# Performance work log

Measured on AMD Instinct MI355X. Metric: run time of the kernel, lower is better.

Reference implementation:

```python
import jax, jax.numpy as jnp
import numpy as np

FWD_W = 1.0
BWD_W = 1.0
EPS = 1e-12  # guard sqrt gradient at exact zero


def setup_inputs() -> dict:
    key = jax.random.key(0)
    k1, k2 = jax.random.split(key)
    pred = jax.random.normal(k1, (4, 8192, 3), dtype=jnp.float32)
    target = jax.random.normal(k2, (4, 8192, 3), dtype=jnp.float32)
    return {"pred": pred, "target": target}


def reference(pred, target):
    # pairwise Euclidean distances (torch.cdist, p=2): (B, N, M)
    sq = (jnp.sum(pred * pred, axis=-1)[:, :, None]
          + jnp.sum(target * target, axis=-1)[:, None, :]
          - 2.0 * jnp.einsum('bnd,bmd->bnm', pred, target))
    dist = jnp.sqrt(jnp.maximum(sq, EPS))
    forward_dist = jnp.min(dist, axis=2)   # (B, N): pred -> nearest target
    backward_dist = jnp.min(dist, axis=1)  # (B, M): target -> nearest pred
    total = FWD_W * jnp.sum(forward_dist, axis=1) + BWD_W * jnp.sum(backward_dist, axis=1)
    return jnp.mean(total)  # reduction='mean'
```

## Files before the change

kernel.cpp:

```cpp
#include <hip/hip_runtime.h>
#include <math.h>

#define BATCH   4
#define NPTS    8192
#define THREADS 256
#define QPT     8
#define QPB     (THREADS * QPT)
#define QBLK    (NPTS / QPB)
#define NSLICE  32
#define SLICE   (NPTS / NSLICE)

typedef float v2f __attribute__((ext_vector_type(2)));

__device__ __forceinline__ v2f pk_fma(v2f a, v2f b, v2f c) {
    v2f d;
    asm("v_pk_fma_f32 %0, %1, %2, %3" : "=v"(d) : "v"(a), "v"(b), "v"(c));
    return d;
}

__global__ __launch_bounds__(THREADS)
void chamfer_min_kernel(const float* __restrict__ pred,
                        const float* __restrict__ target,
                        unsigned int* __restrict__ minbits)
{
    __shared__ float4 sdb[SLICE * 2];

    const int tid = threadIdx.x;
    const int bid = blockIdx.x;
    const int s   = bid & (NSLICE - 1);
    const int qb  = (bid >> 5) & (QBLK - 1);
    const int b   = (bid >> 7) & 3;
    const int dir = bid >> 9;

    const float* __restrict__ qsrc = (dir == 0) ? pred : target;
    const float* __restrict__ dsrc = (dir == 0) ? target : pred;

    {
        const float* dbase = dsrc + ((size_t)b * NPTS + (size_t)s * SLICE) * 3;
        const float x = dbase[3 * tid + 0];
        const float y = dbase[3 * tid + 1];
        const float z = dbase[3 * tid + 2];
        const float w = fmaf(x, x, fmaf(y, y, z * z));
        sdb[2 * tid + 0] = make_float4(-2.0f * x, -2.0f * x, -2.0f * y, -2.0f * y);
        sdb[2 * tid + 1] = make_float4(-2.0f * z, -2.0f * z, w, w);
    }

    v2f qx[4], qy[4], qz[4];
    float qq[QPT];
    {
        const float* qbase = qsrc + ((size_t)b * NPTS + (size_t)qb * QPB) * 3;
        #pragma unroll
        for (int p = 0; p < 4; ++p) {
            const int i0 = (2 * p + 0) * THREADS + tid;
            const int i1 = (2 * p + 1) * THREADS + tid;
            const float x0 = qbase[3 * i0 + 0], y0 = qbase[3 * i0 + 1], z0 = qbase[3 * i0 + 2];
            const float x1 = qbase[3 * i1 + 0], y1 = qbase[3 * i1 + 1], z1 = qbase[3 * i1 + 2];
            qx[p] = (v2f){x0, x1};
            qy[p] = (v2f){y0, y1};
            qz[p] = (v2f){z0, z1};
            qq[2 * p + 0] = fmaf(x0, x0, fmaf(y0, y0, z0 * z0));
            qq[2 * p + 1] = fmaf(x1, x1, fmaf(y1, y1, z1 * z1));
        }
    }

    __syncthreads();

    float mn[QPT];
    #pragma unroll
    for (int i = 0; i < QPT; ++i) mn[i] = 3.0e38f;

    #pragma unroll 2
    for (int j = 0; j < SLICE; j += 2) {
        const float4 c00 = sdb[2 * j + 0];
        const float4 c01 = sdb[2 * j + 1];
        const float4 c10 = sdb[2 * j + 2];
        const float4 c11 = sdb[2 * j + 3];
        const v2f xx0 = (v2f){c00.x, c00.y}, yy0 = (v2f){c00.z, c00.w};
        const v2f zz0 = (v2f){c01.x, c01.y}, ww0 = (v2f){c01.z, c01.w};
        const v2f xx1 = (v2f){c10.x, c10.y}, yy1 = (v2f){c10.z, c10.w};
        const v2f zz1 = (v2f){c11.x, c11.y}, ww1 = (v2f){c11.z, c11.w};

        #pragma unroll
        for (int p = 0; p < 4; ++p) {
            const v2f s0 = pk_fma(qx[p], xx0, pk_fma(qy[p], yy0, pk_fma(qz[p], zz0, ww0)));
            const v2f s1 = pk_fma(qx[p], xx1, pk_fma(qy[p], yy1, pk_fma(qz[p], zz1, ww1)));
            mn[2 * p + 0] = fminf(mn[2 * p + 0], s0.x);
            mn[2 * p + 1] = fminf(mn[2 * p + 1], s0.y);
            mn[2 * p + 0] = fminf(mn[2 * p + 0], s1.x);
            mn[2 * p + 1] = fminf(mn[2 * p + 1], s1.y);
        }
    }

    unsigned int* dst = minbits + (size_t)dir * (BATCH * NPTS)
                                + (size_t)b * NPTS + (size_t)qb * QPB;
    #pragma unroll
    for (int i = 0; i < QPT; ++i) {
        const float sq = fmaxf(qq[i] + mn[i], 1e-12f);
        atomicMin(dst + i * THREADS + tid, __float_as_uint(sq));
    }
}

__global__ __launch_bounds__(1024)
void chamfer_reduce_kernel(const unsigned int* __restrict__ minbits,
                           float* __restrict__ out)
{
    const uint4* p = (const uint4*)minbits;
    float acc = 0.0f;
    #pragma unroll
    for (int k = 0; k < 16; ++k) {
        const uint4 v = p[k * 1024 + threadIdx.x];
        acc += sqrtf(__uint_as_float(v.x)) + sqrtf(__uint_as_float(v.y))
             + sqrtf(__uint_as_float(v.z)) + sqrtf(__uint_as_float(v.w));
    }
    #pragma unroll
    for (int off = 32; off > 0; off >>= 1)
        acc += __shfl_down(acc, off, 64);

    __shared__ float wsum[16];
    const int lane = threadIdx.x & 63;
    const int w    = threadIdx.x >> 6;
    if (lane == 0) wsum[w] = acc;
    __syncthreads();
    if (threadIdx.x == 0) {
        float t = 0.0f;
        #pragma unroll
        for (int k = 0; k < 16; ++k) t += wsum[k];
        out[0] = t * (1.0f / BATCH);
    }
}

extern "C" void kernel_launch(void* const* d_in, const int* in_sizes, int n_in,
                              void* d_out, int out_size, void* d_ws, size_t ws_size,
                              hipStream_t stream)
{
    const float* pred     = (const float*)d_in[0];
    const float* target   = (const float*)d_in[1];
    float* out            = (float*)d_out;
    unsigned int* minbits = (unsigned int*)d_ws;

    const int nblocks = 2 * BATCH * QBLK * NSLICE;
    chamfer_min_kernel<<<nblocks, THREADS, 0, stream>>>(pred, target, minbits);
    chamfer_reduce_kernel<<<1, 1024, 0, stream>>>(minbits, out);
}
```

Before: 102.0 us.

## Widen per-thread query tiles, pack LDS points, replace atomics with partial-min reduction

Each thread now holds 16 query points instead of 8, and the grid uses 64 database slices instead of 32. Each database point is stored as one float4 in LDS, and op_sel variants of v_pk_fma read the broadcast operands directly, with v_min3 merging the candidate distances. The atomicMin writes are replaced by plain stores of per-slice partial minima into a large workspace. Two new kernels then reduce those partials across slices, take square roots and sum them. This removes atomic contention and the serial single-block reduction, at the cost of about 16 MB of workspace traffic, a 64-block reduction pass and higher register pressure.

New measurement: 145.1 us. 42.2% more time.

```diff
diff --git a/kernel.cpp b/kernel.cpp
--- a/kernel.cpp
+++ b/kernel.cpp
@@ -4,53 +4,73 @@
 #define BATCH   4
 #define NPTS    8192
 #define THREADS 256
-#define QPT     8
+#define QPT     16
 #define QPB     (THREADS * QPT)
 #define QBLK    (NPTS / QPB)
-#define NSLICE  32
+#define NSLICE  64
 #define SLICE   (NPTS / NSLICE)
+#define NREGION (2 * BATCH * QBLK)
+#define PART_ELEMS (NREGION * NSLICE * QPB)
 
 typedef float v2f __attribute__((ext_vector_type(2)));
 
-__device__ __forceinline__ v2f pk_fma(v2f a, v2f b, v2f c) {
+
+static __device__ __forceinline__ v2f pk_fma_b_lo(v2f a, v2f b, v2f c) {
     v2f d;
-    asm("v_pk_fma_f32 %0, %1, %2, %3" : "=v"(d) : "v"(a), "v"(b), "v"(c));
+    asm("v_pk_fma_f32 %0, %1, %2, %3 op_sel:[0,0,0] op_sel_hi:[1,0,1]"
+        : "=v"(d) : "v"(a), "v"(b), "v"(c));
+    return d;
+}
+static __device__ __forceinline__ v2f pk_fma_b_hi(v2f a, v2f b, v2f c) {
+    v2f d;
+    asm("v_pk_fma_f32 %0, %1, %2, %3 op_sel:[0,1,0] op_sel_hi:[1,1,1]"
+        : "=v"(d) : "v"(a), "v"(b), "v"(c));
+    return d;
+}
+static __device__ __forceinline__ v2f pk_fma_b_lo_c_hi(v2f a, v2f b, v2f c) {
+    v2f d;
+    asm("v_pk_fma_f32 %0, %1, %2, %3 op_sel:[0,0,1] op_sel_hi:[1,0,1]"
+        : "=v"(d) : "v"(a), "v"(b), "v"(c));
+    return d;
+}
+static __device__ __forceinline__ float min3f(float a, float b, float c) {
+    float d;
+    asm("v_min3_f32 %0, %1, %2, %3" : "=v"(d) : "v"(a), "v"(b), "v"(c));
     return d;
 }
 
 __global__ __launch_bounds__(THREADS)
 void chamfer_min_kernel(const float* __restrict__ pred,
                         const float* __restrict__ target,
-                        unsigned int* __restrict__ minbits)
+                        float* __restrict__ partial)
 {
-    __shared__ float4 sdb[SLICE * 2];
+    __shared__ float4 sdb[SLICE];
 
     const int tid = threadIdx.x;
     const int bid = blockIdx.x;
     const int s   = bid & (NSLICE - 1);
-    const int qb  = (bid >> 5) & (QBLK - 1);
+    const int qb  = (bid >> 6) & (QBLK - 1);
     const int b   = (bid >> 7) & 3;
     const int dir = bid >> 9;
 
     const float* __restrict__ qsrc = (dir == 0) ? pred : target;
     const float* __restrict__ dsrc = (dir == 0) ? target : pred;
 
-    {
+    if (tid < SLICE) {
         const float* dbase = dsrc + ((size_t)b * NPTS + (size_t)s * SLICE) * 3;
         const float x = dbase[3 * tid + 0];
         const float y = dbase[3 * tid + 1];
         const float z = dbase[3 * tid + 2];
-        const float w = fmaf(x, x, fmaf(y, y, z * z));
-        sdb[2 * tid + 0] = make_float4(-2.0f * x, -2.0f * x, -2.0f * y, -2.0f * y);
-        sdb[2 * tid + 1] = make_float4(-2.0f * z, -2.0f * z, w, w);
+        sdb[tid] = make_float4(-2.0f * x, -2.0f * y, -2.0f * z,
+                               fmaf(x, x, fmaf(y, y, z * z)));
     }
 
-    v2f qx[4], qy[4], qz[4];
+    v2f qx[8], qy[8], qz[8];
     float qq[QPT];
     {
         const float* qbase = qsrc + ((size_t)b * NPTS + (size_t)qb * QPB) * 3;
         #pragma unroll
-        for (int p = 0; p < 4; ++p) {
+        for (int p = 0; p < 8; ++p) {
             const int i0 = (2 * p + 0) * THREADS + tid;
             const int i1 = (2 * p + 1) * THREADS + tid;
             const float x0 = qbase[3 * i0 + 0], y0 = qbase[3 * i0 + 1], z0 = qbase[3 * i0 + 2];
@@ -69,76 +89,89 @@
     #pragma unroll
     for (int i = 0; i < QPT; ++i) mn[i] = 3.0e38f;
 
-    #pragma unroll 2
-    for (int j = 0; j < SLICE; j += 2) {
-        const float4 c00 = sdb[2 * j + 0];
-        const float4 c01 = sdb[2 * j + 1];
-        const float4 c10 = sdb[2 * j + 2];
-        const float4 c11 = sdb[2 * j + 3];
-        const v2f xx0 = (v2f){c00.x, c00.y}, yy0 = (v2f){c00.z, c00.w};
-        const v2f zz0 = (v2f){c01.x, c01.y}, ww0 = (v2f){c01.z, c01.w};
-        const v2f xx1 = (v2f){c10.x, c10.y}, yy1 = (v2f){c10.z, c10.w};
-        const v2f zz1 = (v2f){c11.x, c11.y}, ww1 = (v2f){c11.z, c11.w};
+    #pragma unroll 1
+    for (int j = 0; j < SLICE; j += 4) {
+        const float4 d0 = sdb[j + 0];
+        const float4 d1 = sdb[j + 1];
+        const float4 d2 = sdb[j + 2];
+        const float4 d3 = sdb[j + 3];
+        const v2f a0 = (v2f){d0.x, d0.y}, b0 = (v2f){d0.z, d0.w};
+        const v2f a1 = (v2f){d1.x, d1.y}, b1 = (v2f){d1.z, d1.w};
+        const v2f a2 = (v2f){d2.x, d2.y}, b2 = (v2f){d2.z, d2.w};
+        const v2f a3 = (v2f){d3.x, d3.y}, b3 = (v2f){d3.z, d3.w};
 
         #pragma unroll
-        for (int p = 0; p < 4; ++p) {
-            const v2f s0 = pk_fma(qx[p], xx0, pk_fma(qy[p], yy0, pk_fma(qz[p], zz0, ww0)));
-            const v2f s1 = pk_fma(qx[p], xx1, pk_fma(qy[p], yy1, pk_fma(qz[p], zz1, ww1)));
-            mn[2 * p + 0] = fminf(mn[2 * p + 0], s0.x);
-            mn[2 * p + 1] = fminf(mn[2 * p + 1], s0.y);
-            mn[2 * p + 0] = fminf(mn[2 * p + 0], s1.x);
-            mn[2 * p + 1] = fminf(mn[2 * p + 1], s1.y);
+        for (int p = 0; p < 8; ++p) {
+            const v2f s0 = pk_fma_b_lo(qx[p], a0, pk_fma_b_hi(qy[p], a0, pk_fma_b_lo_c_hi(qz[p], b0, b0)));
+            const v2f s1 = pk_fma_b_lo(qx[p], a1, pk_fma_b_hi(qy[p], a1, pk_fma_b_lo_c_hi(qz[p], b1, b1)));
+            const v2f s2 = pk_fma_b_lo(qx[p], a2, pk_fma_b_hi(qy[p], a2, pk_fma_b_lo_c_hi(qz[p], b2, b2)));
+            const v2f s3 = pk_fma_b_lo(qx[p], a3, pk_fma_b_hi(qy[p], a3, pk_fma_b_lo_c_hi(qz[p], b3, b3)));
+            mn[2 * p + 0] = min3f(mn[2 * p + 0], s0.x, s1.x);
+            mn[2 * p + 0] = min3f(mn[2 * p + 0], s2.x, s3.x);
+            mn[2 * p + 1] = min3f(mn[2 * p + 1], s0.y, s1.y);
+            mn[2 * p + 1] = min3f(mn[2 * p + 1], s2.y, s3.y);
         }
     }
 
-    unsigned int* dst = minbits + (size_t)dir * (BATCH * NPTS)
-                                + (size_t)b * NPTS + (size_t)qb * QPB;
+    const int region = ((dir * BATCH + b) * QBLK + qb);
+    float* dst = partial + ((size_t)region * NSLICE + s) * QPB;
     #pragma unroll
     for (int i = 0; i < QPT; ++i) {
-        const float sq = fmaxf(qq[i] + mn[i], 1e-12f);
-        atomicMin(dst + i * THREADS + tid, __float_as_uint(sq));
+        dst[i * THREADS + tid] = fmaxf(qq[i] + mn[i], 1e-12f);
     }
 }
 
-__global__ __launch_bounds__(1024)
-void chamfer_reduce_kernel(const unsigned int* __restrict__ minbits,
-                           float* __restrict__ out)
+__global__ __launch_bounds__(256)
+void chamfer_reduce1(const float* __restrict__ partial,
+                     float* __restrict__ bsum)
 {
-    const uint4* p = (const uint4*)minbits;
+    const int tid = threadIdx.x;
     float acc = 0.0f;
     #pragma unroll
-    for (int k = 0; k < 16; ++k) {
-        const uint4 v = p[k * 1024 + threadIdx.x];
-        acc += sqrtf(__uint_as_float(v.x)) + sqrtf(__uint_as_float(v.y))
-             + sqrtf(__uint_as_float(v.z)) + sqrtf(__uint_as_float(v.w));
+    for (int p = 0; p < 4; ++p) {
+        const int gq     = blockIdx.x * 1024 + p * 256 + tid;
+        const int region = gq >> 12;
+        const int qloc   = gq & (QPB - 1);
+        const float* base = partial + (size_t)region * (NSLICE * QPB) + qloc;
+        float m = base[0];
+        #pragma unroll 8
+        for (int sl = 1; sl < NSLICE; ++sl)
+            m = fminf(m, base[(size_t)sl * QPB]);
+        acc += sqrtf(m);
     }
     #pragma unroll
     for (int off = 32; off > 0; off >>= 1)
         acc += __shfl_down(acc, off, 64);
 
-    __shared__ float wsum[16];
-    const int lane = threadIdx.x & 63;
-    const int w    = threadIdx.x >> 6;
-    if (lane == 0) wsum[w] = acc;
+    __shared__ float wsum[4];
+    if ((tid & 63) == 0) wsum[tid >> 6] = acc;
     __syncthreads();
-    if (threadIdx.x == 0) {
-        float t = 0.0f;
-        #pragma unroll
-        for (int k = 0; k < 16; ++k) t += wsum[k];
-        out[0] = t * (1.0f / BATCH);
-    }
+    if (tid == 0) bsum[blockIdx.x] = wsum[0] + wsum[1] + wsum[2] + wsum[3];
+}
+
+__global__ __launch_bounds__(64)
+void chamfer_reduce2(const float* __restrict__ bsum,
+                     float* __restrict__ out)
+{
+    float v = bsum[threadIdx.x];
+    #pragma unroll
+    for (int off = 32; off > 0; off >>= 1)
+        v += __shfl_down(v, off, 64);
+    if (threadIdx.x == 0) out[0] = v * (1.0f / BATCH);
 }
 
 extern "C" void kernel_launch(void* const* d_in, const int* in_sizes, int n_in,
                               void* d_out, int out_size, void* d_ws, size_t ws_size,
                               hipStream_t stream)
 {
-    const float* pred     = (const float*)d_in[0];
-    const float* target   = (const float*)d_in[1];
-    float* out            = (float*)d_out;
-    unsigned int* minbits = (unsigned int*)d_ws;
+    const float* pred   = (const float*)d_in[0];
+    const float* target = (const float*)d_in[1];
+    float* out          = (float*)d_out;
+    float* partial      = (float*)d_ws;
+    float* bsum         = partial + PART_ELEMS;
 
     const int nblocks = 2 * BATCH * QBLK * NSLICE;
-    chamfer_min_kernel<<<nblocks, THREADS, 0, stream>>>(pred, target, minbits);
-    chamfer_reduce_kernel<<<1, 1024, 0, stream>>>(minbits, out);
+    chamfer_min_kernel<<<nblocks, THREADS, 0, stream>>>(pred, target, partial);
+    chamfer_reduce1<<<64, 256, 0, stream>>>(partial, bsum);
+    chamfer_reduce2<<<1, 64, 0, stream>>>(bsum, out);
 }
```
